# Optimization experiments

Measured on AMD Instinct MI355X. Metric: run time of the kernel, lower is better.

Reference implementation:

```python
import jax, jax.numpy as jnp
import numpy as np

B, S, DIM = 1, 2048, 4096
N_HEADS, N_KV_HEADS = 32, 8
HEAD_DIM = DIM // N_HEADS            # 128
N_REP = N_HEADS // N_KV_HEADS        # 4
Q_SIZE = N_HEADS * HEAD_DIM          # 4096
KV_SIZE = N_KV_HEADS * HEAD_DIM      # 1024


def setup_inputs() -> dict:
    key = jax.random.key(0)
    ks = jax.random.split(key, 5)
    x = jax.random.normal(ks[0], (B, S, DIM), dtype=jnp.float32)
    # RoPE tables: freqs_cis[s, j] = exp(i * s * theta_j), theta_j = 10000^(-2j/head_dim)
    theta = 10000.0 ** (-jnp.arange(0, HEAD_DIM, 2, dtype=jnp.float32) / HEAD_DIM)
    ang = jnp.arange(S, dtype=jnp.float32)[:, None] * theta[None, :]  # [S, HEAD_DIM//2]
    freqs_cos = jnp.cos(ang)
    freqs_sin = jnp.sin(ang)
    # causal additive mask [1,1,S,S]
    causal = jnp.tril(jnp.ones((S, S), dtype=bool))
    mask = jnp.where(causal, 0.0, -1e9).astype(jnp.float32)[None, None]
    wqkv = jax.random.normal(ks[1], (Q_SIZE + 2 * KV_SIZE, DIM), dtype=jnp.float32) * (DIM ** -0.5)
    wo = jax.random.normal(ks[2], (DIM, Q_SIZE), dtype=jnp.float32) * (Q_SIZE ** -0.5)
    return {"x": x, "freqs_cos": freqs_cos, "freqs_sin": freqs_sin, "mask": mask,
            "wqkv": wqkv, "wo": wo}


def _apply_rope(t, cos, sin):
    # t: [B, S, H, D]; cos/sin: [S, D//2]  (complex multiply on (even, odd) pairs)
    b, s, h, d = t.shape
    tp = t.reshape(b, s, h, d // 2, 2)
    t0, t1 = tp[..., 0], tp[..., 1]
    c = cos[None, :, None, :]
    sn = sin[None, :, None, :]
    out = jnp.stack([t0 * c - t1 * sn, t0 * sn + t1 * c], axis=-1)
    return out.reshape(b, s, h, d)


def reference(x, freqs_cos, freqs_sin, mask, wqkv, wo):
    bsz, seqlen, _ = x.shape
    qkv = jnp.einsum('bsd,od->bso', x, wqkv)  # fused QKV projection
    xq = qkv[..., :Q_SIZE].reshape(bsz, seqlen, N_HEADS, HEAD_DIM)
    xk = qkv[..., Q_SIZE:Q_SIZE + KV_SIZE].reshape(bsz, seqlen, N_KV_HEADS, HEAD_DIM)
    xv = qkv[..., Q_SIZE + KV_SIZE:].reshape(bsz, seqlen, N_KV_HEADS, HEAD_DIM)
    # rotary embedding on q, k
    xq = _apply_rope(xq, freqs_cos, freqs_sin)
    xk = _apply_rope(xk, freqs_cos, freqs_sin)
    # cache insertion (prefill: cache == current k/v), layout [B, KVH, S, D]
    cache_k = jnp.swapaxes(xk, 1, 2)
    cache_v = jnp.swapaxes(xv, 1, 2)
    # GQA repeat_kv -> [B, H, S, D]
    keys = jnp.repeat(cache_k, N_REP, axis=1)
    values = jnp.repeat(cache_v, N_REP, axis=1)
    # scores: einsum 'ijkl,ikml->ikjm' with xq [b,s,h,d], keys [b,h,t,d] -> [b,h,s,t]
    scores = jnp.einsum('bshd,bhtd->bhst', xq, keys) / jnp.sqrt(jnp.float32(HEAD_DIM))
    scores = scores + mask
    scores = jax.nn.softmax(scores.astype(jnp.float32), axis=-1).astype(xq.dtype)
    out = jnp.einsum('bhst,bhtd->bhsd', scores, values)  # [B, H, S, D]
    out = jnp.swapaxes(out, 1, 2).reshape(bsz, seqlen, Q_SIZE)
    return jnp.einsum('bso,do->bsd', out, wo)
```

## Files before the change

kernel.cpp:

```cpp
#include <hip/hip_runtime.h>
#include <hip/hip_bf16.h>
#include <cstdint>
#include <cstddef>


typedef __attribute__((ext_vector_type(4)))  float    f32x4;
typedef __attribute__((ext_vector_type(16))) float    f32x16;
typedef __attribute__((ext_vector_type(8)))  __bf16   bf16x8;
typedef __attribute__((ext_vector_type(4)))  __bf16   bf16x4;
typedef __attribute__((ext_vector_type(2)))  __bf16   bf16x2;
typedef __attribute__((ext_vector_type(4)))  uint32_t u32x4;

typedef const __attribute__((address_space(1))) void* gaddr_t;
typedef __attribute__((address_space(3))) void*       laddr_t;

#define S_LEN   2048
#define DIM_    4096
#define NHEADS  32
#define NKV     8
#define HD      128
#define QKV_LD  6144
#define KOFF    4096
#define VOFF    5120

#define EXP2F(x) __builtin_amdgcn_exp2f(x)

__global__ void cvt_f32_bf16(const float* __restrict__ in, __bf16* __restrict__ out, int n4) {
  int idx = blockIdx.x * blockDim.x + threadIdx.x;
  int stride = gridDim.x * blockDim.x;
  for (int i = idx; i < n4; i += stride) {
    float4 v = reinterpret_cast<const float4*>(in)[i];
    bf16x4 o;
    o[0] = (__bf16)v.x; o[1] = (__bf16)v.y; o[2] = (__bf16)v.z; o[3] = (__bf16)v.w;
    reinterpret_cast<bf16x4*>(out)[i] = o;
  }
}

__global__ void rope_kernel(__bf16* __restrict__ qkv, const float* __restrict__ fc,
                            const float* __restrict__ fs) {
  int tid = blockIdx.x * 256 + threadIdx.x;
  int i = tid & 63;
  int t = tid >> 6;
  int h = t % 40;
  int s = t / 40;
  int col = (h < NHEADS) ? (h * HD + 2 * i) : (KOFF + (h - NHEADS) * HD + 2 * i);
  size_t off = (size_t)s * QKV_LD + col;
  float c = fc[s * 64 + i], sn = fs[s * 64 + i];
  bf16x2 v = *reinterpret_cast<bf16x2*>(&qkv[off]);
  float t0 = (float)v[0], t1 = (float)v[1];
  bf16x2 o;
  o[0] = (__bf16)(t0 * c - t1 * sn);
  o[1] = (__bf16)(t0 * sn + t1 * c);
  *reinterpret_cast<bf16x2*>(&qkv[off]) = o;
}

__device__ __forceinline__ void stage64(const __bf16* __restrict__ P, int ld, int row0,
                                        int kt, char* dst, int tid) {
  int r = tid >> 3, g = tid & 7;
  const __bf16* src = P + (size_t)(row0 + r) * ld + kt * 64 + ((g ^ (r & 7)) * 8);
  __builtin_amdgcn_global_load_lds((gaddr_t)src,
      (laddr_t)(dst + (tid & ~63) * 16), 16, 0, 0);
}

template <int MW, int NW, int KH, int NST, bool VM>
__device__ __forceinline__ void phase32(const __bf16* __restrict__ Ab,
                                        const __bf16* __restrict__ Bb,
                                        f32x16 (&acc)[MW][NW],
                                        int wm, int wn, int l31, int hi, int tid,
                                        const __bf16* __restrict__ SP, int sld,
                                        int srow0, char* sdst, int kt, bool st) {
  bf16x8 af[MW][2], bfr[NW][2];
#pragma unroll
  for (int mi = 0; mi < MW; ++mi) {
    int R = wm * (MW * 32) + mi * 32 + l31;
#pragma unroll
    for (int k2 = 0; k2 < 2; ++k2)
      af[mi][k2] = *reinterpret_cast<const bf16x8*>(
          (const char*)Ab + R * 128 + (((KH * 4 + k2 * 2 + hi) ^ (R & 7)) * 16));
  }
#pragma unroll
  for (int ni = 0; ni < NW; ++ni) {
    int R = wn * (NW * 32) + ni * 32 + l31;
#pragma unroll
    for (int k2 = 0; k2 < 2; ++k2)
      bfr[ni][k2] = *reinterpret_cast<const bf16x8*>(
          (const char*)Bb + R * 128 + (((KH * 4 + k2 * 2 + hi) ^ (R & 7)) * 16));
  }
  if (st) {
#pragma unroll
    for (int h = 0; h < NST; ++h)
      stage64(SP, sld, srow0 + h * 64, kt, sdst + h * 8192, tid);
  }
  __builtin_amdgcn_s_barrier();
  asm volatile("s_waitcnt lgkmcnt(0)" ::: "memory");
  __builtin_amdgcn_sched_barrier(0);
  __builtin_amdgcn_s_setprio(1);
#pragma unroll
  for (int k2 = 0; k2 < 2; ++k2)
#pragma unroll
    for (int mi = 0; mi < MW; ++mi)
#pragma unroll
      for (int ni = 0; ni < NW; ++ni)
        acc[mi][ni] = __builtin_amdgcn_mfma_f32_32x32x16_bf16(af[mi][k2], bfr[ni][k2],
                                                              acc[mi][ni], 0, 0, 0);
  __builtin_amdgcn_s_setprio(0);
  if (VM) asm volatile("s_waitcnt vmcnt(0)" ::: "memory");
  __builtin_amdgcn_s_barrier();
}

template <int BM, int BN, int MB, int NPX, typename OutT>
__global__ __launch_bounds__(512, 1) void gemm32(const __bf16* __restrict__ A,
                                                 const __bf16* __restrict__ B,
                                                 OutT* __restrict__ C, int K,
                                                 int lda, int ldb, int ldc) {
  constexpr int MW = BM / 64;
  constexpr int NW = BN / 128;
  constexpr int AST = BM / 64, BST = BN / 64;
  __shared__ __align__(16) __bf16 As[2][BM * 64];
  __shared__ __align__(16) __bf16 Bs[2][BN * 64];
  const int tid = threadIdx.x;
  const int lane = tid & 63, l31 = lane & 31, hi = lane >> 5, w = tid >> 6;
  const int wm = w >> 2, wn = w & 3;
  const int bid = blockIdx.x, xcd = bid & 7, lid = bid >> 3;
  const int m0 = (lid % MB) * BM;
  const int n0 = (xcd * NPX + lid / MB) * BN;

  f32x16 acc[MW][NW] = {};

#pragma unroll
  for (int h = 0; h < AST; ++h) stage64(A, lda, m0 + h * 64, 0, (char*)As[0] + h * 8192, tid);
#pragma unroll
  for (int h = 0; h < BST; ++h) stage64(B, ldb, n0 + h * 64, 0, (char*)Bs[0] + h * 8192, tid);
  asm volatile("s_waitcnt vmcnt(0)" ::: "memory");
  __builtin_amdgcn_s_barrier();

  const int ntiles = K >> 6;
  for (int t = 0; t < ntiles; ++t) {
    const int cur = t & 1;
    const __bf16* Ab = As[cur];
    const __bf16* Bb = Bs[cur];
    char* dA = (char*)As[1 - cur];
    char* dB = (char*)Bs[1 - cur];
    const bool st = (t + 1 < ntiles);
    phase32<MW, NW, 0, AST, false>(Ab, Bb, acc, wm, wn, l31, hi, tid,
                                   A, lda, m0, dA, t + 1, st);
    phase32<MW, NW, 1, BST, true >(Ab, Bb, acc, wm, wn, l31, hi, tid,
                                   B, ldb, n0, dB, t + 1, st);
  }

#pragma unroll
  for (int mi = 0; mi < MW; ++mi)
#pragma unroll
    for (int ni = 0; ni < NW; ++ni)
#pragma unroll
      for (int e = 0; e < 16; ++e) {
        int row = m0 + wm * (MW * 32) + mi * 32 + (e & 3) + 8 * (e >> 2) + 4 * hi;
        int col = n0 + wn * (NW * 32) + ni * 32 + l31;
        C[(size_t)row * ldc + col] = (OutT)acc[mi][ni][e];
      }
}

__device__ inline uint32_t pack2(float a, float b) {
  bf16x2 t; t[0] = (__bf16)a; t[1] = (__bf16)b;
  return __builtin_bit_cast(uint32_t, t);
}

__global__ __launch_bounds__(256, 2) void attn_kernel(const __bf16* __restrict__ qkv,
                                                      __bf16* __restrict__ out) {
  __shared__ __align__(16) __bf16 Ks[2][64 * 128];
  __shared__ __align__(16) __bf16 Vt[2][128][72];
  const int tid = threadIdx.x;
  const int lane = tid & 63, l31 = lane & 31, hi = lane >> 5, wq = tid >> 6;
  const int head = blockIdx.x & 31;
  const int pr = blockIdx.x >> 5;
  const int kvh = head >> 2;
  const float sc2 = 0.08838834764831845f * 1.44269504089f;

  bf16x8 vr[2][2];

  auto stage_k = [&](int tt, int buf) {
#pragma unroll
    for (int i = 0; i < 4; ++i) {
      int c = i * 256 + tid;
      int r = c >> 4, g = c & 15;
      const __bf16* gk = qkv + (size_t)(tt * 64 + r) * QKV_LD + KOFF + kvh * HD + ((g ^ (r & 7)) * 8);
      __builtin_amdgcn_global_load_lds((gaddr_t)gk,
          (laddr_t)((char*)Ks[buf] + (tid & ~63) * 16 + i * 4096), 16, 0, 0);
    }
  };
  auto load_v = [&](int tt) {
#pragma unroll
    for (int i = 0; i < 2; ++i) {
      int task = i * 256 + tid;
      int p = task >> 4, cg = task & 15;
      const __bf16* vp = qkv + (size_t)(tt * 64 + 2 * p) * QKV_LD + VOFF + kvh * HD + cg * 8;
      vr[i][0] = *reinterpret_cast<const bf16x8*>(vp);
      vr[i][1] = *reinterpret_cast<const bf16x8*>(vp + QKV_LD);
    }
  };
  auto write_v = [&](int buf) {
#pragma unroll
    for (int i = 0; i < 2; ++i) {
      int task = i * 256 + tid;
      int p = task >> 4, cg = task & 15;
#pragma unroll
      for (int e0 = 0; e0 < 8; ++e0) {
        int e = e0 ^ (lane & 7);
        bf16x2 pkv; pkv[0] = vr[i][0][e]; pkv[1] = vr[i][1][e];
        *reinterpret_cast<bf16x2*>(&Vt[buf][cg * 8 + e][2 * p]) = pkv;
      }
    }
  };

  for (int pass = 0; pass < 2; ++pass) {
    const int qt = pass ? (15 - pr) : pr;
    const int q0 = qt * 128;
    const int nt = 2 * qt + 2;
    const int qr = q0 + wq * 32 + l31;

    bf16x8 qf[8];
    {
      const __bf16* qp = qkv + (size_t)qr * QKV_LD + head * HD + hi * 8;
#pragma unroll
      for (int ks = 0; ks < 8; ++ks) qf[ks] = *reinterpret_cast<const bf16x8*>(qp + ks * 16);
    }
    f32x16 o[4] = {};
    float m_run = -3e38f, l_run = 0.f;

    __syncthreads();
    stage_k(0, 0); load_v(0); write_v(0);

    for (int t = 0; t < nt; ++t) {
      const int cur = t & 1;
      __syncthreads();
      if (t + 1 < nt) { stage_k(t + 1, 1 - cur); load_v(t + 1); }

      f32x16 st[2];
#pragma unroll
      for (int sub = 0; sub < 2; ++sub) {
        f32x16 acc = {};
        int r = sub * 32 + l31;
#pragma unroll
        for (int ks = 0; ks < 8; ++ks) {
          int g = (ks * 2 + hi) ^ (r & 7);
          bf16x8 kf = *reinterpret_cast<const bf16x8*>((char*)Ks[cur] + r * 256 + g * 16);
          acc = __builtin_amdgcn_mfma_f32_32x32x16_bf16(kf, qf[ks], acc, 0, 0, 0);
        }
        st[sub] = acc;
      }
#pragma unroll
      for (int sub = 0; sub < 2; ++sub)
#pragma unroll
        for (int e = 0; e < 16; ++e) st[sub][e] *= sc2;
      if (t >= nt - 2) {
        const int kv0 = t * 64;
#pragma unroll
        for (int sub = 0; sub < 2; ++sub)
#pragma unroll
          for (int e = 0; e < 16; ++e) {
            int kvg = kv0 + sub * 32 + (e & 3) + 8 * (e >> 2) + 4 * hi;
            if (kvg > qr) st[sub][e] = -1e30f;
          }
      }
      float pm = st[0][0];
#pragma unroll
      for (int e = 1; e < 16; ++e) pm = fmaxf(pm, st[0][e]);
#pragma unroll
      for (int e = 0; e < 16; ++e) pm = fmaxf(pm, st[1][e]);
      pm = fmaxf(pm, __shfl_xor(pm, 32));
      if (!__all(pm - m_run <= 8.f)) {
        float mn = fmaxf(m_run, pm);
        float fsc = EXP2F(m_run - mn);
        m_run = mn;
        l_run *= fsc;
#pragma unroll
        for (int dt = 0; dt < 4; ++dt)
#pragma unroll
          for (int e = 0; e < 16; ++e) o[dt][e] *= fsc;
      }
      float rs = 0.f;
#pragma unroll
      for (int sub = 0; sub < 2; ++sub)
#pragma unroll
        for (int e = 0; e < 16; ++e) {
          float p = EXP2F(st[sub][e] - m_run);
          st[sub][e] = p;
          rs += p;
        }
      rs += __shfl_xor(rs, 32);
      l_run += rs;

      uint32_t pk[16];
#pragma unroll
      for (int sub = 0; sub < 2; ++sub)
#pragma unroll
        for (int i = 0; i < 8; ++i)
          pk[sub * 8 + i] = pack2(st[sub][2 * i], st[sub][2 * i + 1]);
      uint32_t rv[8];
#pragma unroll
      for (int m = 0; m < 8; ++m) {
        int base = 4 * (m >> 1) + (m & 1);
        uint32_t snd = hi ? pk[base] : pk[base + 2];
        rv[m] = __shfl_xor(snd, 32);
      }
      bf16x8 pf[4];
#pragma unroll
      for (int tt = 0; tt < 4; ++tt) {
        u32x4 w;
        w[0] = hi ? rv[2 * tt]     : pk[4 * tt];
        w[1] = hi ? rv[2 * tt + 1] : pk[4 * tt + 1];
        w[2] = hi ? pk[4 * tt + 2] : rv[2 * tt];
        w[3] = hi ? pk[4 * tt + 3] : rv[2 * tt + 1];
        pf[tt] = __builtin_bit_cast(bf16x8, w);
      }
#pragma unroll
      for (int dt = 0; dt < 4; ++dt) {
        int dr = dt * 32 + l31;
#pragma unroll
        for (int tt = 0; tt < 4; ++tt) {
          bf16x8 vf = *reinterpret_cast<const bf16x8*>((char*)&Vt[cur][0][0] + dr * 144 + tt * 32 + hi * 16);
          o[dt] = __builtin_amdgcn_mfma_f32_32x32x16_bf16(vf, pf[tt], o[dt], 0, 0, 0);
        }
      }
      if (t + 1 < nt) write_v(1 - cur);
    }

    float inv = 1.f / l_run;
    __bf16* scr = &Ks[0][0] + wq * 1280;
    const int qq = lane >> 1, part = lane & 1;
#pragma unroll
    for (int dt = 0; dt < 4; ++dt) {
      __syncthreads();
#pragma unroll
      for (int i = 0; i < 8; ++i) {
        int d0 = (2 * i & 3) + 8 * (i >> 1) + 4 * hi;
        bf16x2 prr;
        prr[0] = (__bf16)(o[dt][2 * i] * inv);
        prr[1] = (__bf16)(o[dt][2 * i + 1] * inv);
        *reinterpret_cast<bf16x2*>(scr + l31 * 40 + d0) = prr;
      }
      __syncthreads();
      bf16x8 r0 = *reinterpret_cast<const bf16x8*>(scr + qq * 40 + part * 16);
      bf16x8 r1 = *reinterpret_cast<const bf16x8*>(scr + qq * 40 + part * 16 + 8);
      __bf16* op = out + (size_t)(q0 + wq * 32 + qq) * DIM_ + head * HD + dt * 32 + part * 16;
      *reinterpret_cast<bf16x8*>(op) = r0;
      *reinterpret_cast<bf16x8*>(op + 8) = r1;
    }
  }
}

extern "C" void kernel_launch(void* const* d_in, const int* in_sizes, int n_in,
                              void* d_out, int out_size, void* d_ws, size_t ws_size,
                              hipStream_t stream) {
  (void)in_sizes; (void)n_in; (void)out_size; (void)ws_size;
  const float* x    = (const float*)d_in[0];
  const float* fc   = (const float*)d_in[1];
  const float* fs   = (const float*)d_in[2];
  const float* wqkv = (const float*)d_in[4];
  const float* wo   = (const float*)d_in[5];
  float* out = (float*)d_out;

  char* ws = (char*)d_ws;
  __bf16* xb    = (__bf16*)(ws);
  __bf16* wqkvb = (__bf16*)(ws + 16777216);
  __bf16* wob   = (__bf16*)(ws + 67108864);
  __bf16* qkv   = (__bf16*)(ws + 100663296);
  __bf16* attnO = xb;

  cvt_f32_bf16<<<2048, 256, 0, stream>>>(x,    xb,    (S_LEN * DIM_) / 4);
  cvt_f32_bf16<<<2048, 256, 0, stream>>>(wqkv, wqkvb, (6144 * DIM_) / 4);
  cvt_f32_bf16<<<2048, 256, 0, stream>>>(wo,   wob,   (DIM_ * DIM_) / 4);

  gemm32<256, 256, 8, 3, __bf16><<<192, 512, 0, stream>>>(xb, wqkvb, qkv, DIM_, DIM_, DIM_, QKV_LD);

  rope_kernel<<<(S_LEN * 40 * 64) / 256, 256, 0, stream>>>(qkv, fc, fs);

  attn_kernel<<<256, 256, 0, stream>>>(qkv, attnO);

  gemm32<128, 256, 16, 2, float><<<256, 512, 0, stream>>>(attnO, wob, out, DIM_, DIM_, DIM_, DIM_);
}
```

Baseline: 369.7 us.

## Shrink GEMM tiles to 128x128 and restructure attention into 64-row causal blocks

```diff
diff --git a/kernel.cpp b/kernel.cpp
--- a/kernel.cpp
+++ b/kernel.cpp
@@ -54,42 +54,45 @@
   *reinterpret_cast<bf16x2*>(&qkv[off]) = o;
 }
 
-__device__ __forceinline__ void stage64(const __bf16* __restrict__ P, int ld, int row0,
-                                        int kt, char* dst, int tid) {
-  int r = tid >> 3, g = tid & 7;
-  const __bf16* src = P + (size_t)(row0 + r) * ld + kt * 64 + ((g ^ (r & 7)) * 8);
-  __builtin_amdgcn_global_load_lds((gaddr_t)src,
-      (laddr_t)(dst + (tid & ~63) * 16), 16, 0, 0);
-}
-
-template <int MW, int NW, int KH, int NST, bool VM>
+__device__ __forceinline__ void stage64x(const __bf16* __restrict__ P, int ld, int row0,
+                                         int kt, char* dst, int tid) {
+#pragma unroll
+  for (int j = 0; j < 2; ++j) {
+    int c = j * 256 + tid;
+    int r = c >> 3, g = c & 7;
+    const __bf16* src = P + (size_t)(row0 + r) * ld + kt * 64 + ((g ^ (r & 7)) * 8);
+    __builtin_amdgcn_global_load_lds((gaddr_t)src,
+        (laddr_t)(dst + j * 4096 + (tid & ~63) * 16), 16, 0, 0);
+  }
+}
+
+template <int KH, bool VM>
 __device__ __forceinline__ void phase32(const __bf16* __restrict__ Ab,
                                         const __bf16* __restrict__ Bb,
-                                        f32x16 (&acc)[MW][NW],
+                                        f32x16 (&acc)[2][2],
                                         int wm, int wn, int l31, int hi, int tid,
                                         const __bf16* __restrict__ SP, int sld,
                                         int srow0, char* sdst, int kt, bool st) {
-  bf16x8 af[MW][2], bfr[NW][2];
-#pragma unroll
-  for (int mi = 0; mi < MW; ++mi) {
-    int R = wm * (MW * 32) + mi * 32 + l31;
+  bf16x8 af[2][2], bfr[2][2];
+#pragma unroll
+  for (int mi = 0; mi < 2; ++mi) {
+    int R = wm * 64 + mi * 32 + l31;
 #pragma unroll
     for (int k2 = 0; k2 < 2; ++k2)
       af[mi][k2] = *reinterpret_cast<const bf16x8*>(
           (const char*)Ab + R * 128 + (((KH * 4 + k2 * 2 + hi) ^ (R & 7)) * 16));
   }
 #pragma unroll
-  for (int ni = 0; ni < NW; ++ni) {
-    int R = wn * (NW * 32) + ni * 32 + l31;
+  for (int ni = 0; ni < 2; ++ni) {
+    int R = wn * 64 + ni * 32 + l31;
 #pragma unroll
     for (int k2 = 0; k2 < 2; ++k2)
       bfr[ni][k2] = *reinterpret_cast<const bf16x8*>(
           (const char*)Bb + R * 128 + (((KH * 4 + k2 * 2 + hi) ^ (R & 7)) * 16));
   }
   if (st) {
-#pragma unroll
-    for (int h = 0; h < NST; ++h)
-      stage64(SP, sld, srow0 + h * 64, kt, sdst + h * 8192, tid);
+    stage64x(SP, sld, srow0, kt, sdst, tid);
+    stage64x(SP, sld, srow0 + 64, kt, sdst + 8192, tid);
   }
   __builtin_amdgcn_s_barrier();
   asm volatile("s_waitcnt lgkmcnt(0)" ::: "memory");
@@ -98,9 +101,9 @@
 #pragma unroll
   for (int k2 = 0; k2 < 2; ++k2)
 #pragma unroll
-    for (int mi = 0; mi < MW; ++mi)
-#pragma unroll
-      for (int ni = 0; ni < NW; ++ni)
+    for (int mi = 0; mi < 2; ++mi)
+#pragma unroll
+      for (int ni = 0; ni < 2; ++ni)
         acc[mi][ni] = __builtin_amdgcn_mfma_f32_32x32x16_bf16(af[mi][k2], bfr[ni][k2],
                                                               acc[mi][ni], 0, 0, 0);
   __builtin_amdgcn_s_setprio(0);
@@ -108,29 +111,26 @@
   __builtin_amdgcn_s_barrier();
 }
 
-template <int BM, int BN, int MB, int NPX, typename OutT>
-__global__ __launch_bounds__(512, 1) void gemm32(const __bf16* __restrict__ A,
+template <int MB, int NPX, typename OutT>
+__global__ __launch_bounds__(256, 2) void gemm32(const __bf16* __restrict__ A,
                                                  const __bf16* __restrict__ B,
                                                  OutT* __restrict__ C, int K,
                                                  int lda, int ldb, int ldc) {
-  constexpr int MW = BM / 64;
-  constexpr int NW = BN / 128;
-  constexpr int AST = BM / 64, BST = BN / 64;
-  __shared__ __align__(16) __bf16 As[2][BM * 64];
-  __shared__ __align__(16) __bf16 Bs[2][BN * 64];
+  __shared__ __align__(16) __bf16 As[2][128 * 64];
+  __shared__ __align__(16) __bf16 Bs[2][128 * 64];
   const int tid = threadIdx.x;
   const int lane = tid & 63, l31 = lane & 31, hi = lane >> 5, w = tid >> 6;
-  const int wm = w >> 2, wn = w & 3;
+  const int wm = w >> 1, wn = w & 1;
   const int bid = blockIdx.x, xcd = bid & 7, lid = bid >> 3;
-  const int m0 = (lid % MB) * BM;
-  const int n0 = (xcd * NPX + lid / MB) * BN;
-
-  f32x16 acc[MW][NW] = {};
-
-#pragma unroll
-  for (int h = 0; h < AST; ++h) stage64(A, lda, m0 + h * 64, 0, (char*)As[0] + h * 8192, tid);
-#pragma unroll
-  for (int h = 0; h < BST; ++h) stage64(B, ldb, n0 + h * 64, 0, (char*)Bs[0] + h * 8192, tid);
+  const int m0 = (lid % MB) * 128;
+  const int n0 = (xcd * NPX + lid / MB) * 128;
+
+  f32x16 acc[2][2] = {};
+
+  stage64x(A, lda, m0, 0, (char*)As[0], tid);
+  stage64x(A, lda, m0 + 64, 0, (char*)As[0] + 8192, tid);
+  stage64x(B, ldb, n0, 0, (char*)Bs[0], tid);
+  stage64x(B, ldb, n0 + 64, 0, (char*)Bs[0] + 8192, tid);
   asm volatile("s_waitcnt vmcnt(0)" ::: "memory");
   __builtin_amdgcn_s_barrier();
 
@@ -142,20 +142,18 @@
     char* dA = (char*)As[1 - cur];
     char* dB = (char*)Bs[1 - cur];
     const bool st = (t + 1 < ntiles);
-    phase32<MW, NW, 0, AST, false>(Ab, Bb, acc, wm, wn, l31, hi, tid,
-                                   A, lda, m0, dA, t + 1, st);
-    phase32<MW, NW, 1, BST, true >(Ab, Bb, acc, wm, wn, l31, hi, tid,
-                                   B, ldb, n0, dB, t + 1, st);
-  }
-
-#pragma unroll
-  for (int mi = 0; mi < MW; ++mi)
-#pragma unroll
-    for (int ni = 0; ni < NW; ++ni)
+    phase32<0, false>(Ab, Bb, acc, wm, wn, l31, hi, tid, A, lda, m0, dA, t + 1, st);
+    phase32<1, true >(Ab, Bb, acc, wm, wn, l31, hi, tid, B, ldb, n0, dB, t + 1, st);
+  }
+
+#pragma unroll
+  for (int mi = 0; mi < 2; ++mi)
+#pragma unroll
+    for (int ni = 0; ni < 2; ++ni)
 #pragma unroll
       for (int e = 0; e < 16; ++e) {
-        int row = m0 + wm * (MW * 32) + mi * 32 + (e & 3) + 8 * (e >> 2) + 4 * hi;
-        int col = n0 + wn * (NW * 32) + ni * 32 + l31;
+        int row = m0 + wm * 64 + mi * 32 + (e & 3) + 8 * (e >> 2) + 4 * hi;
+        int col = n0 + wn * 64 + ni * 32 + l31;
         C[(size_t)row * ldc + col] = (OutT)acc[mi][ni][e];
       }
 }
@@ -165,33 +163,26 @@
   return __builtin_bit_cast(uint32_t, t);
 }
 
-__global__ __launch_bounds__(256, 2) void attn_kernel(const __bf16* __restrict__ qkv,
+__global__ __launch_bounds__(128, 2) void attn_kernel(const __bf16* __restrict__ qkv,
                                                       __bf16* __restrict__ out) {
-  __shared__ __align__(16) __bf16 Ks[2][64 * 128];
   __shared__ __align__(16) __bf16 Vt[2][128][72];
   const int tid = threadIdx.x;
   const int lane = tid & 63, l31 = lane & 31, hi = lane >> 5, wq = tid >> 6;
-  const int head = blockIdx.x & 31;
-  const int pr = blockIdx.x >> 5;
+  const int b = blockIdx.x;
+  const int head = b & 31;
+  const int qt = 31 - (b >> 5);
+  const int q0 = qt * 64;
+  const int nt = qt + 1;
   const int kvh = head >> 2;
   const float sc2 = 0.08838834764831845f * 1.44269504089f;
-
-  bf16x8 vr[2][2];
-
-  auto stage_k = [&](int tt, int buf) {
+  const int qr = q0 + wq * 32 + l31;
+
+  bf16x8 vr[4][2];
+
+  auto load_v = [&](int tt) {
 #pragma unroll
     for (int i = 0; i < 4; ++i) {
-      int c = i * 256 + tid;
-      int r = c >> 4, g = c & 15;
-      const __bf16* gk = qkv + (size_t)(tt * 64 + r) * QKV_LD + KOFF + kvh * HD + ((g ^ (r & 7)) * 8);
-      __builtin_amdgcn_global_load_lds((gaddr_t)gk,
-          (laddr_t)((char*)Ks[buf] + (tid & ~63) * 16 + i * 4096), 16, 0, 0);
-    }
-  };
-  auto load_v = [&](int tt) {
-#pragma unroll
-    for (int i = 0; i < 2; ++i) {
-      int task = i * 256 + tid;
+      int task = i * 128 + tid;
       int p = task >> 4, cg = task & 15;
       const __bf16* vp = qkv + (size_t)(tt * 64 + 2 * p) * QKV_LD + VOFF + kvh * HD + cg * 8;
       vr[i][0] = *reinterpret_cast<const bf16x8*>(vp);
@@ -200,8 +191,8 @@
   };
   auto write_v = [&](int buf) {
 #pragma unroll
-    for (int i = 0; i < 2; ++i) {
-      int task = i * 256 + tid;
+    for (int i = 0; i < 4; ++i) {
+      int task = i * 128 + tid;
       int p = task >> 4, cg = task & 15;
 #pragma unroll
       for (int e0 = 0; e0 < 8; ++e0) {
@@ -212,140 +203,133 @@
     }
   };
 
-  for (int pass = 0; pass < 2; ++pass) {
-    const int qt = pass ? (15 - pr) : pr;
-    const int q0 = qt * 128;
-    const int nt = 2 * qt + 2;
-    const int qr = q0 + wq * 32 + l31;
-
-    bf16x8 qf[8];
-    {
-      const __bf16* qp = qkv + (size_t)qr * QKV_LD + head * HD + hi * 8;
-#pragma unroll
-      for (int ks = 0; ks < 8; ++ks) qf[ks] = *reinterpret_cast<const bf16x8*>(qp + ks * 16);
-    }
-    f32x16 o[4] = {};
-    float m_run = -3e38f, l_run = 0.f;
-
+  bf16x8 qf[8];
+  {
+    const __bf16* qp = qkv + (size_t)qr * QKV_LD + head * HD + hi * 8;
+#pragma unroll
+    for (int ks = 0; ks < 8; ++ks) qf[ks] = *reinterpret_cast<const bf16x8*>(qp + ks * 16);
+  }
+  f32x16 o[4] = {};
+  float m_run = -3e38f, l_run = 0.f;
+
+  load_v(0); write_v(0);
+  __syncthreads();
+
+  for (int t = 0; t < nt; ++t) {
+    const int cur = t & 1;
+    if (t + 1 < nt) load_v(t + 1);
+
+    const int kv0 = t * 64;
+    f32x16 st[2];
+#pragma unroll
+    for (int sub = 0; sub < 2; ++sub) {
+      const __bf16* kp = qkv + (size_t)(kv0 + sub * 32 + l31) * QKV_LD + KOFF + kvh * HD + hi * 8;
+      bf16x8 kf[8];
+#pragma unroll
+      for (int ks = 0; ks < 8; ++ks) kf[ks] = *reinterpret_cast<const bf16x8*>(kp + ks * 16);
+      f32x16 acc = {};
+#pragma unroll
+      for (int ks = 0; ks < 8; ++ks)
+        acc = __builtin_amdgcn_mfma_f32_32x32x16_bf16(kf[ks], qf[ks], acc, 0, 0, 0);
+      st[sub] = acc;
+    }
+#pragma unroll
+    for (int sub = 0; sub < 2; ++sub)
+#pragma unroll
+      for (int e = 0; e < 16; ++e) st[sub][e] *= sc2;
+    if (t == nt - 1) {
+#pragma unroll
+      for (int sub = 0; sub < 2; ++sub)
+#pragma unroll
+        for (int e = 0; e < 16; ++e) {
+          int kvg = kv0 + sub * 32 + (e & 3) + 8 * (e >> 2) + 4 * hi;
+          if (kvg > qr) st[sub][e] = -1e30f;
+        }
+    }
+    float pm = st[0][0];
+#pragma unroll
+    for (int e = 1; e < 16; ++e) pm = fmaxf(pm, st[0][e]);
+#pragma unroll
+    for (int e = 0; e < 16; ++e) pm = fmaxf(pm, st[1][e]);
+    pm = fmaxf(pm, __shfl_xor(pm, 32));
+    if (!__all(pm - m_run <= 8.f)) {
+      float mn = fmaxf(m_run, pm);
+      float fsc = EXP2F(m_run - mn);
+      m_run = mn;
+      l_run *= fsc;
+#pragma unroll
+      for (int dt = 0; dt < 4; ++dt)
+#pragma unroll
+        for (int e = 0; e < 16; ++e) o[dt][e] *= fsc;
+    }
+    float rs = 0.f;
+#pragma unroll
+    for (int sub = 0; sub < 2; ++sub)
+#pragma unroll
+      for (int e = 0; e < 16; ++e) {
+        float p = EXP2F(st[sub][e] - m_run);
+        st[sub][e] = p;
+        rs += p;
+      }
+    rs += __shfl_xor(rs, 32);
+    l_run += rs;
+
+    uint32_t pk[16];
+#pragma unroll
+    for (int sub = 0; sub < 2; ++sub)
+#pragma unroll
+      for (int i = 0; i < 8; ++i)
+        pk[sub * 8 + i] = pack2(st[sub][2 * i], st[sub][2 * i + 1]);
+    uint32_t rv[8];
+#pragma unroll
+    for (int m = 0; m < 8; ++m) {
+      int base = 4 * (m >> 1) + (m & 1);
+      uint32_t snd = hi ? pk[base] : pk[base + 2];
+      rv[m] = __shfl_xor(snd, 32);
+    }
+    bf16x8 pf[4];
+#pragma unroll
+    for (int tt = 0; tt < 4; ++tt) {
+      u32x4 wv;
+      wv[0] = hi ? rv[2 * tt]     : pk[4 * tt];
+      wv[1] = hi ? rv[2 * tt + 1] : pk[4 * tt + 1];
+      wv[2] = hi ? pk[4 * tt + 2] : rv[2 * tt];
+      wv[3] = hi ? pk[4 * tt + 3] : rv[2 * tt + 1];
+      pf[tt] = __builtin_bit_cast(bf16x8, wv);
+    }
+#pragma unroll
+    for (int dt = 0; dt < 4; ++dt) {
+      int dr = dt * 32 + l31;
+#pragma unroll
+      for (int tt = 0; tt < 4; ++tt) {
+        bf16x8 vf = *reinterpret_cast<const bf16x8*>((char*)&Vt[cur][0][0] + dr * 144 + tt * 32 + hi * 16);
+        o[dt] = __builtin_amdgcn_mfma_f32_32x32x16_bf16(vf, pf[tt], o[dt], 0, 0, 0);
+      }
+    }
+    if (t + 1 < nt) write_v(1 - cur);
     __syncthreads();
-    stage_k(0, 0); load_v(0); write_v(0);
-
-    for (int t = 0; t < nt; ++t) {
-      const int cur = t & 1;
-      __syncthreads();
-      if (t + 1 < nt) { stage_k(t + 1, 1 - cur); load_v(t + 1); }
-
-      f32x16 st[2];
-#pragma unroll
-      for (int sub = 0; sub < 2; ++sub) {
-        f32x16 acc = {};
-        int r = sub * 32 + l31;
-#pragma unroll
-        for (int ks = 0; ks < 8; ++ks) {
-          int g = (ks * 2 + hi) ^ (r & 7);
-          bf16x8 kf = *reinterpret_cast<const bf16x8*>((char*)Ks[cur] + r * 256 + g * 16);
-          acc = __builtin_amdgcn_mfma_f32_32x32x16_bf16(kf, qf[ks], acc, 0, 0, 0);
-        }
-        st[sub] = acc;
-      }
-#pragma unroll
-      for (int sub = 0; sub < 2; ++sub)
-#pragma unroll
-        for (int e = 0; e < 16; ++e) st[sub][e] *= sc2;
-      if (t >= nt - 2) {
-        const int kv0 = t * 64;
-#pragma unroll
-        for (int sub = 0; sub < 2; ++sub)
-#pragma unroll
-          for (int e = 0; e < 16; ++e) {
-            int kvg = kv0 + sub * 32 + (e & 3) + 8 * (e >> 2) + 4 * hi;
-            if (kvg > qr) st[sub][e] = -1e30f;
-          }
-      }
-      float pm = st[0][0];
-#pragma unroll
-      for (int e = 1; e < 16; ++e) pm = fmaxf(pm, st[0][e]);
-#pragma unroll
-      for (int e = 0; e < 16; ++e) pm = fmaxf(pm, st[1][e]);
-      pm = fmaxf(pm, __shfl_xor(pm, 32));
-      if (!__all(pm - m_run <= 8.f)) {
-        float mn = fmaxf(m_run, pm);
-        float fsc = EXP2F(m_run - mn);
-        m_run = mn;
-        l_run *= fsc;
-#pragma unroll
-        for (int dt = 0; dt < 4; ++dt)
-#pragma unroll
-          for (int e = 0; e < 16; ++e) o[dt][e] *= fsc;
-      }
-      float rs = 0.f;
-#pragma unroll
-      for (int sub = 0; sub < 2; ++sub)
-#pragma unroll
-        for (int e = 0; e < 16; ++e) {
-          float p = EXP2F(st[sub][e] - m_run);
-          st[sub][e] = p;
-          rs += p;
-        }
-      rs += __shfl_xor(rs, 32);
-      l_run += rs;
-
-      uint32_t pk[16];
-#pragma unroll
-      for (int sub = 0; sub < 2; ++sub)
-#pragma unroll
-        for (int i = 0; i < 8; ++i)
-          pk[sub * 8 + i] = pack2(st[sub][2 * i], st[sub][2 * i + 1]);
-      uint32_t rv[8];
-#pragma unroll
-      for (int m = 0; m < 8; ++m) {
-        int base = 4 * (m >> 1) + (m & 1);
-        uint32_t snd = hi ? pk[base] : pk[base + 2];
-        rv[m] = __shfl_xor(snd, 32);
-      }
-      bf16x8 pf[4];
-#pragma unroll
-      for (int tt = 0; tt < 4; ++tt) {
-        u32x4 w;
-        w[0] = hi ? rv[2 * tt]     : pk[4 * tt];
-        w[1] = hi ? rv[2 * tt + 1] : pk[4 * tt + 1];
-        w[2] = hi ? pk[4 * tt + 2] : rv[2 * tt];
-        w[3] = hi ? pk[4 * tt + 3] : rv[2 * tt + 1];
-        pf[tt] = __builtin_bit_cast(bf16x8, w);
-      }
-#pragma unroll
-      for (int dt = 0; dt < 4; ++dt) {
-        int dr = dt * 32 + l31;
-#pragma unroll
-        for (int tt = 0; tt < 4; ++tt) {
-          bf16x8 vf = *reinterpret_cast<const bf16x8*>((char*)&Vt[cur][0][0] + dr * 144 + tt * 32 + hi * 16);
-          o[dt] = __builtin_amdgcn_mfma_f32_32x32x16_bf16(vf, pf[tt], o[dt], 0, 0, 0);
-        }
-      }
-      if (t + 1 < nt) write_v(1 - cur);
-    }
-
-    float inv = 1.f / l_run;
-    __bf16* scr = &Ks[0][0] + wq * 1280;
-    const int qq = lane >> 1, part = lane & 1;
-#pragma unroll
-    for (int dt = 0; dt < 4; ++dt) {
-      __syncthreads();
-#pragma unroll
-      for (int i = 0; i < 8; ++i) {
-        int d0 = (2 * i & 3) + 8 * (i >> 1) + 4 * hi;
-        bf16x2 prr;
-        prr[0] = (__bf16)(o[dt][2 * i] * inv);
-        prr[1] = (__bf16)(o[dt][2 * i + 1] * inv);
-        *reinterpret_cast<bf16x2*>(scr + l31 * 40 + d0) = prr;
-      }
-      __syncthreads();
-      bf16x8 r0 = *reinterpret_cast<const bf16x8*>(scr + qq * 40 + part * 16);
-      bf16x8 r1 = *reinterpret_cast<const bf16x8*>(scr + qq * 40 + part * 16 + 8);
-      __bf16* op = out + (size_t)(q0 + wq * 32 + qq) * DIM_ + head * HD + dt * 32 + part * 16;
-      *reinterpret_cast<bf16x8*>(op) = r0;
-      *reinterpret_cast<bf16x8*>(op + 8) = r1;
-    }
+  }
+
+  float inv = 1.f / l_run;
+  __bf16* scr = (__bf16*)&Vt[0][0][0] + wq * 1280;
+  const int qq = lane >> 1, part = lane & 1;
+#pragma unroll
+  for (int dt = 0; dt < 4; ++dt) {
+    if (dt) __syncthreads();
+#pragma unroll
+    for (int i = 0; i < 8; ++i) {
+      int d0 = (2 * i & 3) + 8 * (i >> 1) + 4 * hi;
+      bf16x2 prr;
+      prr[0] = (__bf16)(o[dt][2 * i] * inv);
+      prr[1] = (__bf16)(o[dt][2 * i + 1] * inv);
+      *reinterpret_cast<bf16x2*>(scr + l31 * 40 + d0) = prr;
+    }
+    __syncthreads();
+    bf16x8 r0 = *reinterpret_cast<const bf16x8*>(scr + qq * 40 + part * 16);
+    bf16x8 r1 = *reinterpret_cast<const bf16x8*>(scr + qq * 40 + part * 16 + 8);
+    __bf16* op = out + (size_t)(q0 + wq * 32 + qq) * DIM_ + head * HD + dt * 32 + part * 16;
+    *reinterpret_cast<bf16x8*>(op) = r0;
+    *reinterpret_cast<bf16x8*>(op + 8) = r1;
   }
 }
 
@@ -371,11 +355,11 @@
   cvt_f32_bf16<<<2048, 256, 0, stream>>>(wqkv, wqkvb, (6144 * DIM_) / 4);
   cvt_f32_bf16<<<2048, 256, 0, stream>>>(wo,   wob,   (DIM_ * DIM_) / 4);
 
-  gemm32<256, 256, 8, 3, __bf16><<<192, 512, 0, stream>>>(xb, wqkvb, qkv, DIM_, DIM_, DIM_, QKV_LD);
+  gemm32<16, 6, __bf16><<<768, 256, 0, stream>>>(xb, wqkvb, qkv, DIM_, DIM_, DIM_, QKV_LD);
 
   rope_kernel<<<(S_LEN * 40 * 64) / 256, 256, 0, stream>>>(qkv, fc, fs);
 
-  attn_kernel<<<256, 256, 0, stream>>>(qkv, attnO);
-
-  gemm32<128, 256, 16, 2, float><<<256, 512, 0, stream>>>(attnO, wob, out, DIM_, DIM_, DIM_, DIM_);
-}
+  attn_kernel<<<1024, 128, 0, stream>>>(qkv, attnO);
+
+  gemm32<16, 4, float><<<512, 256, 0, stream>>>(attnO, wob, out, DIM_, DIM_, DIM_, DIM_);
+}
```

Result: slower. 432.7 us (+17.0%).

## Use 8-phase 16x16 MFMA QKV GEMM and one-tile-per-block attention grid

Applied to the files above, without the earlier changes.

```diff
diff --git a/kernel.cpp b/kernel.cpp
--- a/kernel.cpp
+++ b/kernel.cpp
@@ -54,12 +54,138 @@
   *reinterpret_cast<bf16x2*>(&qkv[off]) = o;
 }
 
-__device__ __forceinline__ void stage64(const __bf16* __restrict__ P, int ld, int row0,
-                                        int kt, char* dst, int tid) {
+__device__ __forceinline__ void stg64(const __bf16* __restrict__ P, int ld, int row0,
+                                      int kt, char* dst, int tid) {
   int r = tid >> 3, g = tid & 7;
-  const __bf16* src = P + (size_t)(row0 + r) * ld + kt * 64 + ((g ^ (r & 7)) * 8);
+  int row = row0 + r;
+  const __bf16* src = P + (size_t)row * ld + kt * 64 + ((g ^ (row & 7)) * 8);
   __builtin_amdgcn_global_load_lds((gaddr_t)src,
       (laddr_t)(dst + (tid & ~63) * 16), 16, 0, 0);
+}
+
+template <int QM, int QN, bool RA, bool RB, int VW>
+__device__ __forceinline__ void g1_phase(const __bf16* __restrict__ Ab,
+                                         const __bf16* __restrict__ Bb,
+                                         f32x4 (&acc)[8][4],
+                                         bf16x8 (&afr)[4][2], bf16x8 (&bfr)[2][2],
+                                         int wm, int wn, int l15, int hi, int tid,
+                                         const __bf16* __restrict__ SP, int sld,
+                                         int srow, int skt, char* sdst, bool doSt) {
+  if constexpr (RA) {
+#pragma unroll
+    for (int fm = 0; fm < 4; ++fm) {
+      int R = wm * 128 + QM * 64 + fm * 16 + l15;
+#pragma unroll
+      for (int kk = 0; kk < 2; ++kk)
+        afr[fm][kk] = *reinterpret_cast<const bf16x8*>(
+            (const char*)Ab + R * 128 + (((kk * 4 + hi) ^ (R & 7)) * 16));
+    }
+  }
+  if constexpr (RB) {
+#pragma unroll
+    for (int fn = 0; fn < 2; ++fn) {
+      int R = wn * 64 + QN * 32 + fn * 16 + l15;
+#pragma unroll
+      for (int kk = 0; kk < 2; ++kk)
+        bfr[fn][kk] = *reinterpret_cast<const bf16x8*>(
+            (const char*)Bb + R * 128 + (((kk * 4 + hi) ^ (R & 7)) * 16));
+    }
+  }
+  if (doSt) {
+    stg64(SP, sld, srow, skt, sdst, tid);
+    stg64(SP, sld, srow + 64, skt, sdst + 8192, tid);
+  }
+  __builtin_amdgcn_s_barrier();
+  asm volatile("s_waitcnt lgkmcnt(0)" ::: "memory");
+  __builtin_amdgcn_sched_barrier(0);
+  __builtin_amdgcn_s_setprio(1);
+#pragma unroll
+  for (int kk = 0; kk < 2; ++kk)
+#pragma unroll
+    for (int fm = 0; fm < 4; ++fm)
+#pragma unroll
+      for (int fn = 0; fn < 2; ++fn)
+        acc[QM * 4 + fm][QN * 2 + fn] = __builtin_amdgcn_mfma_f32_16x16x32_bf16(
+            afr[fm][kk], bfr[fn][kk], acc[QM * 4 + fm][QN * 2 + fn], 0, 0, 0);
+  __builtin_amdgcn_s_setprio(0);
+  if constexpr (VW == 4) asm volatile("s_waitcnt vmcnt(4)" ::: "memory");
+  if constexpr (VW == 0) asm volatile("s_waitcnt vmcnt(0)" ::: "memory");
+  __builtin_amdgcn_s_barrier();
+}
+
+__global__ __launch_bounds__(512) void g1_8p(const __bf16* __restrict__ A,
+                                             const __bf16* __restrict__ B,
+                                             __bf16* __restrict__ C, int K,
+                                             int lda, int ldb, int ldc) {
+  __shared__ __align__(16) __bf16 As[2][256 * 64];
+  __shared__ __align__(16) __bf16 Bs[2][256 * 64];
+  const int tid = threadIdx.x;
+  const int l15 = tid & 15, hi = (tid >> 4) & 3, w = tid >> 6;
+  const int wm = w >> 2, wn = w & 3;
+  const int bid = blockIdx.x, xcd = bid & 7, lid = bid >> 3;
+  const int m0 = (lid % 8) * 256;
+  const int n0 = (xcd * 3 + lid / 8) * 256;
+
+  f32x4 acc[8][4] = {};
+  bf16x8 afr[4][2], bfr[2][2];
+  char* A0 = (char*)As[0]; char* A1 = (char*)As[1];
+  char* B0 = (char*)Bs[0]; char* B1 = (char*)Bs[1];
+
+  stg64(A, lda, m0,       0, A0,         tid); stg64(A, lda, m0 + 64,  0, A0 + 8192,  tid);
+  stg64(B, ldb, n0,       0, B0,         tid); stg64(B, ldb, n0 + 64,  0, B0 + 8192,  tid);
+  stg64(A, lda, m0 + 128, 0, A0 + 16384, tid); stg64(A, lda, m0 + 192, 0, A0 + 24576, tid);
+  stg64(B, ldb, n0 + 128, 0, B0 + 16384, tid); stg64(B, ldb, n0 + 192, 0, B0 + 24576, tid);
+  stg64(A, lda, m0,       1, A1,         tid); stg64(A, lda, m0 + 64,  1, A1 + 8192,  tid);
+  stg64(B, ldb, n0 + 128, 1, B1 + 16384, tid); stg64(B, ldb, n0 + 192, 1, B1 + 24576, tid);
+  asm volatile("s_waitcnt vmcnt(4)" ::: "memory");
+  __builtin_amdgcn_s_barrier();
+
+  const int nt = K >> 6;
+  for (int it = 0; it < nt; it += 2) {
+    const bool sB = (it + 2 < nt), sC = (it + 3 < nt);
+    const bool last = !sB;
+    const __bf16* Ab0 = As[0]; const __bf16* Bb0 = Bs[0];
+    const __bf16* Ab1 = As[1]; const __bf16* Bb1 = Bs[1];
+    g1_phase<0, 0, true,  true, -1>(Ab0, Bb0, acc, afr, bfr, wm, wn, l15, hi, tid,
+                                    A, lda, m0 + 128, it + 1, A1 + 16384, true);
+    g1_phase<0, 1, false, true, -1>(Ab0, Bb0, acc, afr, bfr, wm, wn, l15, hi, tid,
+                                    B, ldb, n0, it + 1, B1, true);
+    g1_phase<1, 1, true, false, -1>(Ab0, Bb0, acc, afr, bfr, wm, wn, l15, hi, tid,
+                                    A, lda, m0, it + 2, A0, sB);
+    if (last)
+      g1_phase<1, 0, false, true, 0>(Ab0, Bb0, acc, afr, bfr, wm, wn, l15, hi, tid,
+                                     B, ldb, n0 + 128, it + 2, B0 + 16384, sB);
+    else
+      g1_phase<1, 0, false, true, 4>(Ab0, Bb0, acc, afr, bfr, wm, wn, l15, hi, tid,
+                                     B, ldb, n0 + 128, it + 2, B0 + 16384, sB);
+    g1_phase<0, 0, true,  true, -1>(Ab1, Bb1, acc, afr, bfr, wm, wn, l15, hi, tid,
+                                    A, lda, m0 + 128, it + 2, A0 + 16384, sB);
+    g1_phase<0, 1, false, true, -1>(Ab1, Bb1, acc, afr, bfr, wm, wn, l15, hi, tid,
+                                    B, ldb, n0, it + 2, B0, sB);
+    g1_phase<1, 1, true, false, -1>(Ab1, Bb1, acc, afr, bfr, wm, wn, l15, hi, tid,
+                                    A, lda, m0, it + 3, A1, sC);
+    if (last)
+      g1_phase<1, 0, false, true, 0>(Ab1, Bb1, acc, afr, bfr, wm, wn, l15, hi, tid,
+                                     B, ldb, n0 + 128, it + 3, B1 + 16384, sC);
+    else
+      g1_phase<1, 0, false, true, 4>(Ab1, Bb1, acc, afr, bfr, wm, wn, l15, hi, tid,
+                                     B, ldb, n0 + 128, it + 3, B1 + 16384, sC);
+  }
+
+#pragma unroll
+  for (int qm = 0; qm < 2; ++qm)
+#pragma unroll
+    for (int fm = 0; fm < 4; ++fm)
+#pragma unroll
+      for (int qn = 0; qn < 2; ++qn)
+#pragma unroll
+        for (int fn = 0; fn < 2; ++fn)
+#pragma unroll
+          for (int j = 0; j < 4; ++j) {
+            int row = m0 + wm * 128 + qm * 64 + fm * 16 + hi * 4 + j;
+            int col = n0 + wn * 64 + qn * 32 + fn * 16 + l15;
+            C[(size_t)row * ldc + col] = (__bf16)acc[qm * 4 + fm][qn * 2 + fn][j];
+          }
 }
 
 template <int MW, int NW, int KH, int NST, bool VM>
@@ -89,7 +215,7 @@
   if (st) {
 #pragma unroll
     for (int h = 0; h < NST; ++h)
-      stage64(SP, sld, srow0 + h * 64, kt, sdst + h * 8192, tid);
+      stg64(SP, sld, srow0 + h * 64, kt, sdst + h * 8192, tid);
   }
   __builtin_amdgcn_s_barrier();
   asm volatile("s_waitcnt lgkmcnt(0)" ::: "memory");
@@ -109,10 +235,10 @@
 }
 
 template <int BM, int BN, int MB, int NPX, typename OutT>
-__global__ __launch_bounds__(512, 1) void gemm32(const __bf16* __restrict__ A,
-                                                 const __bf16* __restrict__ B,
-                                                 OutT* __restrict__ C, int K,
-                                                 int lda, int ldb, int ldc) {
+__global__ __launch_bounds__(512) void gemm32(const __bf16* __restrict__ A,
+                                              const __bf16* __restrict__ B,
+                                              OutT* __restrict__ C, int K,
+                                              int lda, int ldb, int ldc) {
   constexpr int MW = BM / 64;
   constexpr int NW = BN / 128;
   constexpr int AST = BM / 64, BST = BN / 64;
@@ -128,9 +254,9 @@
   f32x16 acc[MW][NW] = {};
 
 #pragma unroll
-  for (int h = 0; h < AST; ++h) stage64(A, lda, m0 + h * 64, 0, (char*)As[0] + h * 8192, tid);
-#pragma unroll
-  for (int h = 0; h < BST; ++h) stage64(B, ldb, n0 + h * 64, 0, (char*)Bs[0] + h * 8192, tid);
+  for (int h = 0; h < AST; ++h) stg64(A, lda, m0 + h * 64, 0, (char*)As[0] + h * 8192, tid);
+#pragma unroll
+  for (int h = 0; h < BST; ++h) stg64(B, ldb, n0 + h * 64, 0, (char*)Bs[0] + h * 8192, tid);
   asm volatile("s_waitcnt vmcnt(0)" ::: "memory");
   __builtin_amdgcn_s_barrier();
 
@@ -172,9 +298,13 @@
   const int tid = threadIdx.x;
   const int lane = tid & 63, l31 = lane & 31, hi = lane >> 5, wq = tid >> 6;
   const int head = blockIdx.x & 31;
-  const int pr = blockIdx.x >> 5;
+  const int g = blockIdx.x >> 5;
+  const int qt = (g < 8) ? (15 - g) : (g - 8);
+  const int q0 = qt * 128;
+  const int nt = 2 * qt + 2;
   const int kvh = head >> 2;
   const float sc2 = 0.08838834764831845f * 1.44269504089f;
+  const int qr = q0 + wq * 32 + l31;
 
   bf16x8 vr[2][2];
 
@@ -182,8 +312,8 @@
 #pragma unroll
     for (int i = 0; i < 4; ++i) {
       int c = i * 256 + tid;
-      int r = c >> 4, g = c & 15;
-      const __bf16* gk = qkv + (size_t)(tt * 64 + r) * QKV_LD + KOFF + kvh * HD + ((g ^ (r & 7)) * 8);
+      int r = c >> 4, gg = c & 15;
+      const __bf16* gk = qkv + (size_t)(tt * 64 + r) * QKV_LD + KOFF + kvh * HD + ((gg ^ (r & 7)) * 8);
       __builtin_amdgcn_global_load_lds((gaddr_t)gk,
           (laddr_t)((char*)Ks[buf] + (tid & ~63) * 16 + i * 4096), 16, 0, 0);
     }
@@ -212,140 +342,132 @@
     }
   };
 
-  for (int pass = 0; pass < 2; ++pass) {
-    const int qt = pass ? (15 - pr) : pr;
-    const int q0 = qt * 128;
-    const int nt = 2 * qt + 2;
-    const int qr = q0 + wq * 32 + l31;
-
-    bf16x8 qf[8];
-    {
-      const __bf16* qp = qkv + (size_t)qr * QKV_LD + head * HD + hi * 8;
-#pragma unroll
-      for (int ks = 0; ks < 8; ++ks) qf[ks] = *reinterpret_cast<const bf16x8*>(qp + ks * 16);
-    }
-    f32x16 o[4] = {};
-    float m_run = -3e38f, l_run = 0.f;
-
+  bf16x8 qf[8];
+  {
+    const __bf16* qp = qkv + (size_t)qr * QKV_LD + head * HD + hi * 8;
+#pragma unroll
+    for (int ks = 0; ks < 8; ++ks) qf[ks] = *reinterpret_cast<const bf16x8*>(qp + ks * 16);
+  }
+  f32x16 o[4] = {};
+  float m_run = -3e38f, l_run = 0.f;
+
+  stage_k(0, 0); load_v(0); write_v(0);
+
+  for (int t = 0; t < nt; ++t) {
+    const int cur = t & 1;
     __syncthreads();
-    stage_k(0, 0); load_v(0); write_v(0);
-
-    for (int t = 0; t < nt; ++t) {
-      const int cur = t & 1;
-      __syncthreads();
-      if (t + 1 < nt) { stage_k(t + 1, 1 - cur); load_v(t + 1); }
-
-      f32x16 st[2];
-#pragma unroll
-      for (int sub = 0; sub < 2; ++sub) {
-        f32x16 acc = {};
-        int r = sub * 32 + l31;
-#pragma unroll
-        for (int ks = 0; ks < 8; ++ks) {
-          int g = (ks * 2 + hi) ^ (r & 7);
-          bf16x8 kf = *reinterpret_cast<const bf16x8*>((char*)Ks[cur] + r * 256 + g * 16);
-          acc = __builtin_amdgcn_mfma_f32_32x32x16_bf16(kf, qf[ks], acc, 0, 0, 0);
+    if (t + 1 < nt) { stage_k(t + 1, 1 - cur); load_v(t + 1); }
+
+    f32x16 st[2];
+#pragma unroll
+    for (int sub = 0; sub < 2; ++sub) {
+      f32x16 acc = {};
+      int r = sub * 32 + l31;
+#pragma unroll
+      for (int ks = 0; ks < 8; ++ks) {
+        int gg = (ks * 2 + hi) ^ (r & 7);
+        bf16x8 kf = *reinterpret_cast<const bf16x8*>((char*)Ks[cur] + r * 256 + gg * 16);
+        acc = __builtin_amdgcn_mfma_f32_32x32x16_bf16(kf, qf[ks], acc, 0, 0, 0);
+      }
+      st[sub] = acc;
+    }
+#pragma unroll
+    for (int sub = 0; sub < 2; ++sub)
+#pragma unroll
+      for (int e = 0; e < 16; ++e) st[sub][e] *= sc2;
+    if (t >= nt - 2) {
+      const int kv0 = t * 64;
+#pragma unroll
+      for (int sub = 0; sub < 2; ++sub)
+#pragma unroll
+        for (int e = 0; e < 16; ++e) {
+          int kvg = kv0 + sub * 32 + (e & 3) + 8 * (e >> 2) + 4 * hi;
+          if (kvg > qr) st[sub][e] = -1e30f;
         }
-        st[sub] = acc;
+    }
+    float pm = st[0][0];
+#pragma unroll
+    for (int e = 1; e < 16; ++e) pm = fmaxf(pm, st[0][e]);
+#pragma unroll
+    for (int e = 0; e < 16; ++e) pm = fmaxf(pm, st[1][e]);
+    pm = fmaxf(pm, __shfl_xor(pm, 32));
+    if (!__all(pm - m_run <= 8.f)) {
+      float mn = fmaxf(m_run, pm);
+      float fsc = EXP2F(m_run - mn);
+      m_run = mn;
+      l_run *= fsc;
+#pragma unroll
+      for (int dt = 0; dt < 4; ++dt)
+#pragma unroll
+        for (int e = 0; e < 16; ++e) o[dt][e] *= fsc;
+    }
+    float rs = 0.f;
+#pragma unroll
+    for (int sub = 0; sub < 2; ++sub)
+#pragma unroll
+      for (int e = 0; e < 16; ++e) {
+        float p = EXP2F(st[sub][e] - m_run);
+        st[sub][e] = p;
+        rs += p;
       }
-#pragma unroll
-      for (int sub = 0; sub < 2; ++sub)
-#pragma unroll
-        for (int e = 0; e < 16; ++e) st[sub][e] *= sc2;
-      if (t >= nt - 2) {
-        const int kv0 = t * 64;
-#pragma unroll
-        for (int sub = 0; sub < 2; ++sub)
-#pragma unroll
-          for (int e = 0; e < 16; ++e) {
-            int kvg = kv0 + sub * 32 + (e & 3) + 8 * (e >> 2) + 4 * hi;
-            if (kvg > qr) st[sub][e] = -1e30f;
-          }
+    rs += __shfl_xor(rs, 32);
+    l_run += rs;
+
+    uint32_t pk[16];
+#pragma unroll
+    for (int sub = 0; sub < 2; ++sub)
+#pragma unroll
+      for (int i = 0; i < 8; ++i)
+        pk[sub * 8 + i] = pack2(st[sub][2 * i], st[sub][2 * i + 1]);
+    uint32_t rv[8];
+#pragma unroll
+    for (int m = 0; m < 8; ++m) {
+      int base = 4 * (m >> 1) + (m & 1);
+      uint32_t snd = hi ? pk[base] : pk[base + 2];
+      rv[m] = __shfl_xor(snd, 32);
+    }
+    bf16x8 pf[4];
+#pragma unroll
+    for (int tt = 0; tt < 4; ++tt) {
+      u32x4 wv;
+      wv[0] = hi ? rv[2 * tt]     : pk[4 * tt];
+      wv[1] = hi ? rv[2 * tt + 1] : pk[4 * tt + 1];
+      wv[2] = hi ? pk[4 * tt + 2] : rv[2 * tt];
+      wv[3] = hi ? pk[4 * tt + 3] : rv[2 * tt + 1];
+      pf[tt] = __builtin_bit_cast(bf16x8, wv);
+    }
+#pragma unroll
+    for (int dt = 0; dt < 4; ++dt) {
+      int dr = dt * 32 + l31;
+#pragma unroll
+      for (int tt = 0; tt < 4; ++tt) {
+        bf16x8 vf = *reinterpret_cast<const bf16x8*>((char*)&Vt[cur][0][0] + dr * 144 + tt * 32 + hi * 16);
+        o[dt] = __builtin_amdgcn_mfma_f32_32x32x16_bf16(vf, pf[tt], o[dt], 0, 0, 0);
       }
-      float pm = st[0][0];
-#pragma unroll
-      for (int e = 1; e < 16; ++e) pm = fmaxf(pm, st[0][e]);
-#pragma unroll
-      for (int e = 0; e < 16; ++e) pm = fmaxf(pm, st[1][e]);
-      pm = fmaxf(pm, __shfl_xor(pm, 32));
-      if (!__all(pm - m_run <= 8.f)) {
-        float mn = fmaxf(m_run, pm);
-        float fsc = EXP2F(m_run - mn);
-        m_run = mn;
-        l_run *= fsc;
-#pragma unroll
-        for (int dt = 0; dt < 4; ++dt)
-#pragma unroll
-          for (int e = 0; e < 16; ++e) o[dt][e] *= fsc;
-      }
-      float rs = 0.f;
-#pragma unroll
-      for (int sub = 0; sub < 2; ++sub)
-#pragma unroll
-        for (int e = 0; e < 16; ++e) {
-          float p = EXP2F(st[sub][e] - m_run);
-          st[sub][e] = p;
-          rs += p;
-        }
-      rs += __shfl_xor(rs, 32);
-      l_run += rs;
-
-      uint32_t pk[16];
-#pragma unroll
-      for (int sub = 0; sub < 2; ++sub)
-#pragma unroll
-        for (int i = 0; i < 8; ++i)
-          pk[sub * 8 + i] = pack2(st[sub][2 * i], st[sub][2 * i + 1]);
-      uint32_t rv[8];
-#pragma unroll
-      for (int m = 0; m < 8; ++m) {
-        int base = 4 * (m >> 1) + (m & 1);
-        uint32_t snd = hi ? pk[base] : pk[base + 2];
-        rv[m] = __shfl_xor(snd, 32);
-      }
-      bf16x8 pf[4];
-#pragma unroll
-      for (int tt = 0; tt < 4; ++tt) {
-        u32x4 w;
-        w[0] = hi ? rv[2 * tt]     : pk[4 * tt];
-        w[1] = hi ? rv[2 * tt + 1] : pk[4 * tt + 1];
-        w[2] = hi ? pk[4 * tt + 2] : rv[2 * tt];
-        w[3] = hi ? pk[4 * tt + 3] : rv[2 * tt + 1];
-        pf[tt] = __builtin_bit_cast(bf16x8, w);
-      }
-#pragma unroll
-      for (int dt = 0; dt < 4; ++dt) {
-        int dr = dt * 32 + l31;
-#pragma unroll
-        for (int tt = 0; tt < 4; ++tt) {
-          bf16x8 vf = *reinterpret_cast<const bf16x8*>((char*)&Vt[cur][0][0] + dr * 144 + tt * 32 + hi * 16);
-          o[dt] = __builtin_amdgcn_mfma_f32_32x32x16_bf16(vf, pf[tt], o[dt], 0, 0, 0);
-        }
-      }
-      if (t + 1 < nt) write_v(1 - cur);
-    }
-
-    float inv = 1.f / l_run;
-    __bf16* scr = &Ks[0][0] + wq * 1280;
-    const int qq = lane >> 1, part = lane & 1;
-#pragma unroll
-    for (int dt = 0; dt < 4; ++dt) {
-      __syncthreads();
-#pragma unroll
-      for (int i = 0; i < 8; ++i) {
-        int d0 = (2 * i & 3) + 8 * (i >> 1) + 4 * hi;
-        bf16x2 prr;
-        prr[0] = (__bf16)(o[dt][2 * i] * inv);
-        prr[1] = (__bf16)(o[dt][2 * i + 1] * inv);
-        *reinterpret_cast<bf16x2*>(scr + l31 * 40 + d0) = prr;
-      }
-      __syncthreads();
-      bf16x8 r0 = *reinterpret_cast<const bf16x8*>(scr + qq * 40 + part * 16);
-      bf16x8 r1 = *reinterpret_cast<const bf16x8*>(scr + qq * 40 + part * 16 + 8);
-      __bf16* op = out + (size_t)(q0 + wq * 32 + qq) * DIM_ + head * HD + dt * 32 + part * 16;
-      *reinterpret_cast<bf16x8*>(op) = r0;
-      *reinterpret_cast<bf16x8*>(op + 8) = r1;
-    }
+    }
+    if (t + 1 < nt) write_v(1 - cur);
+  }
+
+  float inv = 1.f / l_run;
+  __bf16* scr = &Ks[0][0] + wq * 1280;
+  const int qq = lane >> 1, part = lane & 1;
+#pragma unroll
+  for (int dt = 0; dt < 4; ++dt) {
+    __syncthreads();
+#pragma unroll
+    for (int i = 0; i < 8; ++i) {
+      int d0 = (2 * i & 3) + 8 * (i >> 1) + 4 * hi;
+      bf16x2 prr;
+      prr[0] = (__bf16)(o[dt][2 * i] * inv);
+      prr[1] = (__bf16)(o[dt][2 * i + 1] * inv);
+      *reinterpret_cast<bf16x2*>(scr + l31 * 40 + d0) = prr;
+    }
+    __syncthreads();
+    bf16x8 r0 = *reinterpret_cast<const bf16x8*>(scr + qq * 40 + part * 16);
+    bf16x8 r1 = *reinterpret_cast<const bf16x8*>(scr + qq * 40 + part * 16 + 8);
+    __bf16* op = out + (size_t)(q0 + wq * 32 + qq) * DIM_ + head * HD + dt * 32 + part * 16;
+    *reinterpret_cast<bf16x8*>(op) = r0;
+    *reinterpret_cast<bf16x8*>(op + 8) = r1;
   }
 }
 
@@ -371,11 +493,11 @@
   cvt_f32_bf16<<<2048, 256, 0, stream>>>(wqkv, wqkvb, (6144 * DIM_) / 4);
   cvt_f32_bf16<<<2048, 256, 0, stream>>>(wo,   wob,   (DIM_ * DIM_) / 4);
 
-  gemm32<256, 256, 8, 3, __bf16><<<192, 512, 0, stream>>>(xb, wqkvb, qkv, DIM_, DIM_, DIM_, QKV_LD);
+  g1_8p<<<192, 512, 0, stream>>>(xb, wqkvb, qkv, DIM_, DIM_, DIM_, QKV_LD);
 
   rope_kernel<<<(S_LEN * 40 * 64) / 256, 256, 0, stream>>>(qkv, fc, fs);
 
-  attn_kernel<<<256, 256, 0, stream>>>(qkv, attnO);
+  attn_kernel<<<512, 256, 0, stream>>>(qkv, attnO);
 
   gemm32<128, 256, 16, 2, float><<<256, 512, 0, stream>>>(attnO, wob, out, DIM_, DIM_, DIM_, DIM_);
 }
```

Measured after the change: 357.2 us. -3.4%, faster.
